# Kernel tuning notes

Hardware: AMD Instinct MI355X
Metric: run time of the kernel (lower is better)

Reference implementation:

```python
import jax, jax.numpy as jnp
import numpy as np

B, N, L = 32, 128, 1024
DRUG_DIM, TGT_DIM, HID, H = 256, 1280, 512, 8
HD = HID // H  # 64
NEG = jnp.float32(-1e9)


def setup_inputs() -> dict:
    key = jax.random.key(0)
    ks = jax.random.split(key, 9)
    drug_nodes = jax.random.normal(ks[0], (B, N, DRUG_DIM), dtype=jnp.float32)
    target_seq = jax.random.normal(ks[1], (B, L, TGT_DIM), dtype=jnp.float32)
    # masks: random valid lengths in [max//2, max], True = valid
    dlen = jax.random.randint(ks[2], (B,), N // 2, N + 1)
    tlen = jax.random.randint(ks[3], (B,), L // 2, L + 1)
    drug_mask = jnp.arange(N)[None, :] < dlen[:, None]
    target_mask = jnp.arange(L)[None, :] < tlen[:, None]
    # params (nn.Linear default init ~ U(-1/sqrt(fan_in), ...); randn*0.02 ok for a reference)
    Wd = jax.random.normal(ks[4], (DRUG_DIM, HID), dtype=jnp.float32) / np.sqrt(DRUG_DIM)
    bd = jnp.zeros((HID,), dtype=jnp.float32)
    Wt = jax.random.normal(ks[5], (TGT_DIM, HID), dtype=jnp.float32) / np.sqrt(TGT_DIM)
    bt = jnp.zeros((HID,), dtype=jnp.float32)
    Wb = jax.random.normal(ks[6], (H, HD, HD), dtype=jnp.float32) * 0.02
    return {"drug_nodes": drug_nodes, "drug_mask": drug_mask,
            "target_seq": target_seq, "target_mask": target_mask,
            "Wd": Wd, "bd": bd, "Wt": Wt, "bt": bt, "Wb": Wb}


def reference(drug_nodes, drug_mask, target_seq, target_mask, Wd, bd, Wt, bt, Wb):
    # project and split heads -> (h, B, n, hd) / (h, B, l, hd)
    d = drug_nodes @ Wd + bd                                  # (B, N, HID)
    t = target_seq @ Wt + bt                                  # (B, L, HID)
    dh = d.reshape(B, N, H, HD).transpose(2, 0, 1, 3)         # (H, B, N, HD)
    th = t.reshape(B, L, H, HD).transpose(2, 0, 1, 3)         # (H, B, L, HD)

    dW = jnp.einsum('hbnd,hde->hbne', dh, Wb)                 # bilinear map
    attn = jnp.einsum('hbne,hble->hbnl', dW, th)              # (H, B, N, L)

    mask = (drug_mask[:, :, None] & target_mask[:, None, :])[None]  # (1, B, N, L)
    scores = jnp.where(mask, attn, NEG)

    # drug-side softmax over protein residues (axis=-1), dropout is identity (eval)
    attn_d = jnp.where(mask, jax.nn.softmax(scores, axis=-1), 0.0)
    ctx_d = jnp.einsum('hbnl,hble->hbne', attn_d, th)         # (H, B, N, HD)
    dmf = drug_mask[None, :, :, None].astype(ctx_d.dtype)
    ctx_d = (ctx_d * dmf).sum(axis=2) / jnp.clip(dmf.sum(axis=2), 1.0)  # (H, B, HD)
    ctx_d = ctx_d.transpose(1, 0, 2).reshape(B, -1)           # (B, HID)

    # target-side softmax over atoms (axis=-2)
    attn_t = jnp.where(mask, jax.nn.softmax(scores, axis=-2), 0.0)
    ctx_t = jnp.einsum('hbnl,hbne->hble', attn_t, dh)         # (H, B, L, HD)
    tmf = target_mask[None, :, :, None].astype(ctx_t.dtype)
    ctx_t = (ctx_t * tmf).sum(axis=2) / jnp.clip(tmf.sum(axis=2), 1.0)  # (H, B, HD)
    ctx_t = ctx_t.transpose(1, 0, 2).reshape(B, -1)           # (B, HID)

    return jnp.concatenate([ctx_d, ctx_t], axis=-1)           # (B, 2*HID)
```

## Files before the change

### kernel.cpp

```cpp
#include <hip/hip_runtime.h>
#include <hip/hip_bf16.h>
#include <math.h>

#define B_ 32
#define N_ 128
#define L_ 1024
#define DD_ 256
#define TD_ 1280
#define HID_ 512
#define H_ 8
#define HD_ 64

#define WS_D    0
#define WS_RM   (WS_D   + 2097152)
#define WS_RIZ  (WS_RM  + 32768)
#define WS_RMT  (WS_RIZ + 32768)
#define WS_RZT  (WS_RMT + 524288)
#define WS_RWT  (WS_RZT + 524288)
#define WS_CNT  (WS_RWT + 524288)
#define WS_WT   (WS_CNT + 64)
#define WS_THB  (WS_WT  + 327680)
#define WS_DWB  (WS_THB + 8388608)

using bf16x8 = __attribute__((ext_vector_type(8))) short;
using u16x4 = __attribute__((ext_vector_type(4))) unsigned short;
using floatx4 = __attribute__((ext_vector_type(4))) float;

static __device__ __forceinline__ unsigned short f2bf(float f) {
  unsigned int u = __float_as_uint(f);
  unsigned int r = (u + 0x7FFFu + ((u >> 16) & 1u)) >> 16;
  return (unsigned short)r;
}
static __device__ __forceinline__ float bf2f(unsigned short s) {
  return __uint_as_float(((unsigned int)s) << 16);
}
static __device__ __forceinline__ void gload16(const void* g, void* l) {
  __builtin_amdgcn_global_load_lds(
      (const __attribute__((address_space(1))) void*)g,
      (__attribute__((address_space(3))) void*)l, 16, 0, 0);
}

__global__ __launch_bounds__(256) void count_kernel(const int* __restrict__ dmask,
                                                    const int* __restrict__ tmask,
                                                    int* __restrict__ cnts) {
  __shared__ int red[256];
  const int b = blockIdx.x, tid = threadIdx.x;
  const bool dint = (dmask[0] == 1);
  const bool tint = (tmask[0] == 1);
  int s = 0;
  if (dint) {
    for (int i = tid; i < N_; i += 256) s += (dmask[(size_t)b*N_ + i] != 0);
  } else {
    const unsigned char* p = (const unsigned char*)dmask;
    for (int i = tid; i < N_; i += 256) s += (p[(size_t)b*N_ + i] != 0);
  }
  red[tid] = s; __syncthreads();
  for (int off = 128; off > 0; off >>= 1) { if (tid < off) red[tid] += red[tid+off]; __syncthreads(); }
  if (tid == 0) cnts[b*2] = red[0];
  __syncthreads();
  s = 0;
  if (tint) {
    for (int i = tid; i < L_; i += 256) s += (tmask[(size_t)b*L_ + i] != 0);
  } else {
    const unsigned char* p = (const unsigned char*)tmask;
    for (int i = tid; i < L_; i += 256) s += (p[(size_t)b*L_ + i] != 0);
  }
  red[tid] = s; __syncthreads();
  for (int off = 128; off > 0; off >>= 1) { if (tid < off) red[tid] += red[tid+off]; __syncthreads(); }
  if (tid == 0) cnts[b*2+1] = red[0];
}

__global__ __launch_bounds__(256) void transpose_bf16_kernel(
    const float* __restrict__ W, unsigned short* __restrict__ WT, int K, int Nd) {
  __shared__ float tile[32][33];
  const int tid = threadIdx.x;
  const int n0 = blockIdx.x * 32, k0 = blockIdx.y * 32;
  const int c = tid & 31, r0 = tid >> 5;
#pragma unroll
  for (int i = 0; i < 4; i++) {
    const int r = r0 + i * 8;
    tile[c][r] = W[(size_t)(k0 + r) * Nd + n0 + c];
  }
  __syncthreads();
#pragma unroll
  for (int i = 0; i < 4; i++) {
    const int r = r0 + i * 8;
    WT[(size_t)(n0 + r) * K + k0 + c] = f2bf(tile[r][c]);
  }
}

__global__ __launch_bounds__(256, 2) void gemm_t_mfma_kernel(
    const float* __restrict__ A, const unsigned short* __restrict__ WT,
    const float* __restrict__ bias, unsigned short* __restrict__ thb, int K) {
  __shared__ __align__(16) unsigned short As[8192];
  __shared__ __align__(16) unsigned short Bs[16384];
  const int tid = threadIdx.x;
  const int lin = blockIdx.x;
  const int xcd = lin & 7, sq = lin >> 3;
  const int n_t = sq & 1, m_t = (sq >> 1) + xcd * 32;
  const int m0 = m_t * 128, n0 = n_t * 256;
  const int lane = tid & 63, wave = tid >> 6;
  const int wm = wave & 1, wn = wave >> 1;
  const int quad = lane >> 4, lrow = lane & 15;

  floatx4 acc[4][8];
#pragma unroll
  for (int i = 0; i < 4; i++)
#pragma unroll
    for (int j = 0; j < 8; j++) acc[i][j] = (floatx4){0.f, 0.f, 0.f, 0.f};

  int srcoffB[4][2];
#pragma unroll
  for (int call = 0; call < 4; call++) {
    const int i = call * 256 + tid;
    const int r = i >> 2;
    const int c = (i & 3) ^ ((r >> 1) & 3);
#pragma unroll
    for (int g = 0; g < 2; g++) srcoffB[call][g] = r * K + g * 32 + c * 8;
  }

  const int arow_ = wave * 4 + (lane >> 4);
  const int x_ = lane & 15;
  const int ag_ = x_ >> 3;
  const int acq_ = (x_ & 7) >> 1;
  const int ahalf_ = x_ & 1;

  const float* Abase = A + (size_t)m0 * K;
  const unsigned short* Bbase = WT + (size_t)n0 * K;

  float4 apf[8];

  auto aload = [&](int k0) {
#pragma unroll
    for (int i = 0; i < 8; i++)
      apf[i] = *(const float4*)(Abase + (size_t)(i * 16 + arow_) * K + k0 + x_ * 4);
  };
  auto awrite = [&]() {
#pragma unroll
    for (int i = 0; i < 8; i++) {
      const int r = i * 16 + arow_;
      const int sw = (r >> 1) & 3;
      u16x4 p;
      p[0] = f2bf(apf[i].x); p[1] = f2bf(apf[i].y);
      p[2] = f2bf(apf[i].z); p[3] = f2bf(apf[i].w);
      *(u16x4*)&As[ag_ * 4096 + (r * 4 + (acq_ ^ sw)) * 8 + ahalf_ * 4] = p;
    }
  };
  auto bstage = [&](int k0) {
#pragma unroll
    for (int g = 0; g < 2; g++)
#pragma unroll
      for (int call = 0; call < 4; call++) {
        const int dst = g * 8192 + (call * 256 + wave * 64) * 8;
        gload16(Bbase + k0 + srcoffB[call][g], &Bs[dst]);
      }
  };

  const int nkt = K / 64;
  aload(0);

  for (int t = 0; t < nkt; t++) {
    __syncthreads();
    bstage(t * 64);
    awrite();
    __syncthreads();
    if (t + 1 < nkt) aload((t + 1) * 64);
#pragma unroll
    for (int g = 0; g < 2; g++) {
      bf16x8 afr[4];
#pragma unroll
      for (int i = 0; i < 4; i++) {
        const int ar = wm * 64 + i * 16 + lrow;
        afr[i] = *(const bf16x8*)&As[g * 4096 + (ar * 4 + (quad ^ ((ar >> 1) & 3))) * 8];
      }
#pragma unroll
      for (int jh = 0; jh < 2; jh++) {
        bf16x8 bfr[4];
#pragma unroll
        for (int j = 0; j < 4; j++) {
          const int br = wn * 128 + (jh * 4 + j) * 16 + lrow;
          bfr[j] = *(const bf16x8*)&Bs[g * 8192 + (br * 4 + (quad ^ ((br >> 1) & 3))) * 8];
        }
#pragma unroll
        for (int i = 0; i < 4; i++)
#pragma unroll
          for (int j = 0; j < 4; j++)
            acc[i][jh * 4 + j] = __builtin_amdgcn_mfma_f32_16x16x32_bf16(
                afr[i], bfr[j], acc[i][jh * 4 + j], 0, 0, 0);
      }
    }
  }

  float bj[8];
#pragma unroll
  for (int j = 0; j < 8; j++) bj[j] = bias[n0 + wn * 128 + j * 16 + lrow];
#pragma unroll
  for (int i = 0; i < 4; i++) {
#pragma unroll
    for (int j = 0; j < 8; j++) {
      const int gcol = n0 + wn * 128 + j * 16 + lrow;
      const int hh = gcol >> 6, e = gcol & 63;
#pragma unroll
      for (int r = 0; r < 4; r++) {
        const int grow = m0 + wm * 64 + i * 16 + quad * 4 + r;
        const int bb = grow >> 10, l = grow & 1023;
        thb[(((size_t)bb * H_ + hh) * L_ + l) * HD_ + e] = f2bf(acc[i][j][r] + bj[j]);
      }
    }
  }
}

__global__ __launch_bounds__(256) void gemm_bias_kernel(
    const float* __restrict__ A, const float* __restrict__ W,
    const float* __restrict__ bias, float* __restrict__ C,
    int M, int K, int Nd) {
  __shared__ float As[8][132];
  __shared__ float Bs[8][132];
  const int tid = threadIdx.x;
  const int m0 = blockIdx.y * 128, n0 = blockIdx.x * 128;
  const int lr = tid >> 1, lc = (tid & 1) * 4;
  const int wr = tid >> 5, wc = (tid & 31) * 4;
  const int tm = (tid >> 4) * 4, tn = (tid & 15) * 4;

  float acc[2][2][4][4];
#pragma unroll
  for (int a = 0; a < 2; a++)
#pragma unroll
    for (int bq = 0; bq < 2; bq++)
#pragma unroll
      for (int i = 0; i < 4; i++)
#pragma unroll
        for (int j = 0; j < 4; j++) acc[a][bq][i][j] = 0.f;

  const float* Aptr = A + (size_t)(m0 + lr) * K + lc;
  const float* Wptr = W + (size_t)wr * Nd + n0 + wc;

  for (int k0 = 0; k0 < K; k0 += 8) {
    float4 a4 = *(const float4*)(Aptr + k0);
    float4 w4 = *(const float4*)(Wptr + (size_t)k0 * Nd);
    __syncthreads();
    As[lc+0][lr] = a4.x; As[lc+1][lr] = a4.y; As[lc+2][lr] = a4.z; As[lc+3][lr] = a4.w;
    *(float4*)&Bs[wr][wc] = w4;
    __syncthreads();
#pragma unroll
    for (int kk = 0; kk < 8; kk++) {
      float4 a0 = *(const float4*)&As[kk][tm];
      float4 a1 = *(const float4*)&As[kk][tm + 64];
      float4 b0 = *(const float4*)&Bs[kk][tn];
      float4 b1 = *(const float4*)&Bs[kk][tn + 64];
      const float av0[4] = {a0.x, a0.y, a0.z, a0.w};
      const float av1[4] = {a1.x, a1.y, a1.z, a1.w};
      const float bv0[4] = {b0.x, b0.y, b0.z, b0.w};
      const float bv1[4] = {b1.x, b1.y, b1.z, b1.w};
#pragma unroll
      for (int i = 0; i < 4; i++)
#pragma unroll
        for (int j = 0; j < 4; j++) {
          acc[0][0][i][j] += av0[i] * bv0[j];
          acc[0][1][i][j] += av0[i] * bv1[j];
          acc[1][0][i][j] += av1[i] * bv0[j];
          acc[1][1][i][j] += av1[i] * bv1[j];
        }
    }
  }
  float4 bias0 = *(const float4*)&bias[n0 + tn];
  float4 bias1 = *(const float4*)&bias[n0 + tn + 64];
  const float bb0[4] = {bias0.x, bias0.y, bias0.z, bias0.w};
  const float bb1[4] = {bias1.x, bias1.y, bias1.z, bias1.w};
#pragma unroll
  for (int mh = 0; mh < 2; mh++)
#pragma unroll
    for (int i = 0; i < 4; i++) {
      const int row = m0 + mh * 64 + tm + i;
      float* cp = C + (size_t)row * Nd + n0;
      float4 o0, o1;
      o0.x = acc[mh][0][i][0] + bb0[0]; o0.y = acc[mh][0][i][1] + bb0[1];
      o0.z = acc[mh][0][i][2] + bb0[2]; o0.w = acc[mh][0][i][3] + bb0[3];
      o1.x = acc[mh][1][i][0] + bb1[0]; o1.y = acc[mh][1][i][1] + bb1[1];
      o1.z = acc[mh][1][i][2] + bb1[2]; o1.w = acc[mh][1][i][3] + bb1[3];
      *(float4*)(cp + tn) = o0;
      *(float4*)(cp + tn + 64) = o1;
    }
}

__global__ __launch_bounds__(256) void dw_kernel(
    const float* __restrict__ dproj, const float* __restrict__ Wb,
    unsigned short* __restrict__ dWb) {
  __shared__ float wb_s[64 * 64];
  __shared__ float dp_s[128 * 64];
  const int tid = threadIdx.x;
  const int hb = blockIdx.x, b = hb >> 3, h = hb & 7;
  for (int i = tid; i < 4096; i += 256) wb_s[i] = Wb[(size_t)h * 4096 + i];
#pragma unroll
  for (int rep = 0; rep < 8; rep++) {
    const int idx = rep * 256 + tid;
    const int row = idx >> 4, c4 = (idx & 15) * 4;
    *(float4*)&dp_s[row * 64 + c4] =
        *(const float4*)&dproj[((size_t)(b * N_ + row)) * HID_ + h * HD_ + c4];
  }
  __syncthreads();
  const int n = tid >> 1, half = tid & 1;
  float acc[32];
#pragma unroll
  for (int e = 0; e < 32; e++) acc[e] = 0.f;
  const float* dpr = &dp_s[n * 64];
  for (int k = 0; k < 64; k++) {
    const float a = dpr[k];
    const float* wr = &wb_s[k * 64 + half * 32];
#pragma unroll
    for (int e4 = 0; e4 < 8; e4++) {
      float4 w = *(const float4*)&wr[e4 * 4];
      acc[e4*4+0] += a * w.x; acc[e4*4+1] += a * w.y;
      acc[e4*4+2] += a * w.z; acc[e4*4+3] += a * w.w;
    }
  }
  unsigned short* outp = dWb + ((size_t)hb * N_ + n) * HD_ + half * 32;
#pragma unroll
  for (int e = 0; e < 32; e++) outp[e] = f2bf(acc[e]);
}

__device__ __forceinline__ void mfma_S_tile(
    const unsigned short* __restrict__ thp, const unsigned short* __restrict__ dwp,
    float* __restrict__ S_s, int ncnt, int lv, int tid) {
  const int lane = tid & 63, wave = tid >> 6;
  const int quad = lane >> 4, lr = lane & 15;
  const int noff = (wave & 1) * 64, loff = (wave >> 1) * 32;

  floatx4 acc[4][2];
#pragma unroll
  for (int i = 0; i < 4; i++)
#pragma unroll
    for (int j = 0; j < 2; j++) acc[i][j] = (floatx4){0.f, 0.f, 0.f, 0.f};

#pragma unroll
  for (int kc = 0; kc < 2; kc++) {
    bf16x8 bfr[2];
#pragma unroll
    for (int j = 0; j < 2; j++)
      bfr[j] = *(const bf16x8*)&thp[(size_t)(loff + j * 16 + lr) * HD_ + kc * 32 + quad * 8];
#pragma unroll
    for (int i = 0; i < 4; i++) {
      bf16x8 afr = *(const bf16x8*)&dwp[(size_t)(noff + i * 16 + lr) * HD_ + kc * 32 + quad * 8];
#pragma unroll
      for (int j = 0; j < 2; j++)
        acc[i][j] = __builtin_amdgcn_mfma_f32_16x16x32_bf16(afr, bfr[j], acc[i][j], 0, 0, 0);
    }
  }
#pragma unroll
  for (int i = 0; i < 4; i++)
#pragma unroll
    for (int j = 0; j < 2; j++)
#pragma unroll
      for (int r = 0; r < 4; r++) {
        const int n = noff + i * 16 + quad * 4 + r;
        const int li = loff + j * 16 + lr;
        const bool ok = (n < ncnt) && (li < lv);
        S_s[n * 69 + li] = ok ? acc[i][j][r] : -1e9f;
      }
}

__global__ __launch_bounds__(256, 4) void attn_stats_kernel(
    const unsigned short* __restrict__ thb, const unsigned short* __restrict__ dWb,
    const int* __restrict__ cnts, float* __restrict__ rwt,
    float* __restrict__ rmt, float* __restrict__ rzt) {
  __shared__ float S_s[128 * 69];
  __shared__ float red[256];
  __shared__ float zb_s[256], wb_s[256];
  __shared__ float cm_s[64], ics_s[64];
  const int tid = threadIdx.x;
  const int hb = blockIdx.x >> 4, lt = blockIdx.x & 15;
  const int b = hb >> 3;
  const int ncnt = cnts[b * 2], lcnt = cnts[b * 2 + 1];
  const int l0g = lt * 64;
  if (l0g >= lcnt) return;
  const int lv = min(64, lcnt - l0g);

  mfma_S_tile(thb + ((size_t)hb * L_ + l0g) * HD_, dWb + (size_t)hb * N_ * HD_,
              S_s, ncnt, lv, tid);
  __syncthreads();

  {
    const int l = tid & 63, q = tid >> 6;
    const int ne = min(q * 32 + 32, ncnt);
    float pm = -INFINITY;
    for (int n = q * 32; n < ne; n++) pm = fmaxf(pm, S_s[n * 69 + l]);
    red[tid] = pm;
  }
  __syncthreads();
  if (tid < 64)
    cm_s[tid] = fmaxf(fmaxf(red[tid], red[tid + 64]), fmaxf(red[tid + 128], red[tid + 192]));
  __syncthreads();
  {
    const int l = tid & 63, q = tid >> 6;
    const int ne = min(q * 32 + 32, ncnt);
    const float cm = cm_s[l];
    float ps = 0.f;
    for (int n = q * 32; n < ne; n++) ps += __expf(S_s[n * 69 + l] - cm);
    red[tid] = ps;
  }
  __syncthreads();
  if (tid < 64)
    ics_s[tid] = 1.f / (red[tid] + red[tid + 64] + red[tid + 128] + red[tid + 192]);
  __syncthreads();
  {
    const int n = tid & 127, half = tid >> 7;
    const float* Sr = &S_s[n * 69];
    const int lb = half * 32, le = min(lb + 32, lv);
    float tmax = -INFINITY;
    for (int l = lb; l < le; l++) tmax = fmaxf(tmax, Sr[l]);
    red[tid] = tmax;
    __syncthreads();
    const float tm = fmaxf(red[n], red[n + 128]);
    float z = 0.f, w = 0.f;
    for (int l = lb; l < le; l++) {
      const float s = Sr[l];
      z += __expf(s - tm);
      w += __expf(s - cm_s[l]) * ics_s[l];
    }
    zb_s[tid] = z; wb_s[tid] = w;
    __syncthreads();
    if (tid < 128) {
      const size_t o = ((size_t)hb * 16 + lt) * 128 + tid;
      rmt[o] = tm;
      rzt[o] = zb_s[tid] + zb_s[tid + 128];
      rwt[o] = wb_s[tid] + wb_s[tid + 128];
    }
  }
}

__global__ __launch_bounds__(256) void attn_combine_kernel(
    const float* __restrict__ rmt, const float* __restrict__ rzt,
    const float* __restrict__ rwt, const float* __restrict__ dproj,
    const int* __restrict__ cnts, float* __restrict__ rm_g,
    float* __restrict__ riz_g, float* __restrict__ outp) {
  __shared__ float red[256];
  __shared__ float w_s[128];
  const int tid = threadIdx.x;
  const int hb = blockIdx.x, b = hb >> 3, h = hb & 7;
  const int ncnt = cnts[b * 2], lcnt = cnts[b * 2 + 1];
  const int ntl = (lcnt + 63) >> 6;
  if (tid < 128) {
    const int n = tid;
    float m = -INFINITY;
    for (int t = 0; t < ntl; t++)
      m = fmaxf(m, rmt[((size_t)hb * 16 + t) * 128 + n]);
    float Z = 0.f, w = 0.f;
    for (int t = 0; t < ntl; t++) {
      const size_t o = ((size_t)hb * 16 + t) * 128 + n;
      Z += rzt[o] * __expf(rmt[o] - m);
      w += rwt[o];
    }
    rm_g[hb * 128 + n] = m;
    riz_g[hb * 128 + n] = (n < ncnt) ? 1.f / Z : 0.f;
    w_s[n] = (n < ncnt) ? w : 0.f;
  }
  __syncthreads();
  const int e = tid & 63, q = tid >> 6;
  float p = 0.f;
  const int nb = q * 32, ne = min(nb + 32, ncnt);
  for (int n = nb; n < ne; n++)
    p += w_s[n] * dproj[((size_t)(b * N_ + n)) * HID_ + h * HD_ + e];
  red[tid] = p;
  __syncthreads();
  if (tid < 64) {
    const float s = red[tid] + red[tid + 64] + red[tid + 128] + red[tid + 192];
    outp[(size_t)b * (2 * HID_) + HID_ + h * HD_ + tid] = s / (float)lcnt;
  }
}

__global__ __launch_bounds__(256, 4) void attn_v_kernel(
    const unsigned short* __restrict__ thb, const unsigned short* __restrict__ dWb,
    const int* __restrict__ cnts, const float* __restrict__ rm_g,
    const float* __restrict__ riz_g, float* __restrict__ outp) {
  __shared__ float S_s[128 * 69];
  __shared__ float red[256];
  __shared__ float rm_s[128], riz_s[128], v_s[64];
  const int tid = threadIdx.x;
  const int hb = blockIdx.x >> 4, lt = blockIdx.x & 15;
  const int b = hb >> 3, h = hb & 7;
  const int ncnt = cnts[b * 2], lcnt = cnts[b * 2 + 1];
  const int l0g = lt * 64;
  if (l0g >= lcnt) return;
  const int lv = min(64, lcnt - l0g);

  if (tid < 128) {
    rm_s[tid] = rm_g[hb * 128 + tid];
    riz_s[tid] = riz_g[hb * 128 + tid];
  }
  const unsigned short* thp = thb + ((size_t)hb * L_ + l0g) * HD_;
  mfma_S_tile(thp, dWb + (size_t)hb * N_ * HD_, S_s, ncnt, lv, tid);
  __syncthreads();

  {
    const int l = tid & 63, q = tid >> 6;
    const int ne = min(q * 32 + 32, ncnt);
    float vp = 0.f;
    for (int n = q * 32; n < ne; n++)
      vp += __expf(S_s[n * 69 + l] - rm_s[n]) * riz_s[n];
    red[tid] = vp;
  }
  __syncthreads();
  const float incnt = 1.f / (float)ncnt;
  if (tid < 64) {
    const float v = (tid < lv)
        ? (red[tid] + red[tid + 64] + red[tid + 128] + red[tid + 192]) * incnt
        : 0.f;
    v_s[tid] = v;
  }
  __syncthreads();
  {
    const int e = tid & 63, q = tid >> 6;
    const int le = min(q * 16 + 16, lv);
    float p = 0.f;
    for (int l = q * 16; l < le; l++)
      p += v_s[l] * bf2f(thp[(size_t)l * HD_ + e]);
    red[tid] = p;
  }
  __syncthreads();
  if (tid < 64) {
    const float s = red[tid] + red[tid + 64] + red[tid + 128] + red[tid + 192];
    if (s != 0.f)
      atomicAdd(&outp[(size_t)b * (2 * HID_) + h * HD_ + tid], s);
  }
}

extern "C" void kernel_launch(void* const* d_in, const int* in_sizes, int n_in,
                              void* d_out, int out_size, void* d_ws, size_t ws_size,
                              hipStream_t stream) {
  const float* drug = (const float*)d_in[0];
  const int* dmask = (const int*)d_in[1];
  const float* tseq = (const float*)d_in[2];
  const int* tmask = (const int*)d_in[3];
  const float* Wd = (const float*)d_in[4];
  const float* bd = (const float*)d_in[5];
  const float* Wt = (const float*)d_in[6];
  const float* bt = (const float*)d_in[7];
  const float* Wb = (const float*)d_in[8];
  float* out = (float*)d_out;
  float* ws = (float*)d_ws;

  float* dp = ws + WS_D;
  float* rm = ws + WS_RM;
  float* riz = ws + WS_RIZ;
  float* rmt = ws + WS_RMT;
  float* rzt = ws + WS_RZT;
  float* rwt = ws + WS_RWT;
  int* cnts = (int*)(ws + WS_CNT);
  unsigned short* wtT = (unsigned short*)(ws + WS_WT);
  unsigned short* thb = (unsigned short*)(ws + WS_THB);
  unsigned short* dWb = (unsigned short*)(ws + WS_DWB);

  count_kernel<<<B_, 256, 0, stream>>>(dmask, tmask, cnts);
  hipMemsetAsync(out, 0, (size_t)out_size * sizeof(float), stream);
  transpose_bf16_kernel<<<dim3(HID_ / 32, TD_ / 32), 256, 0, stream>>>(Wt, wtT, TD_, HID_);
  gemm_t_mfma_kernel<<<(HID_ / 256) * ((B_ * L_) / 128), 256, 0, stream>>>(
      tseq, wtT, bt, thb, TD_);
  gemm_bias_kernel<<<dim3(HID_ / 128, (B_ * N_) / 128), 256, 0, stream>>>(
      drug, Wd, bd, dp, B_ * N_, DD_, HID_);
  dw_kernel<<<B_ * H_, 256, 0, stream>>>(dp, Wb, dWb);
  attn_stats_kernel<<<B_ * H_ * 16, 256, 0, stream>>>(thb, dWb, cnts, rwt, rmt, rzt);
  attn_combine_kernel<<<B_ * H_, 256, 0, stream>>>(rmt, rzt, rwt, dp, cnts, rm, riz, out);
  attn_v_kernel<<<B_ * H_ * 16, 256, 0, stream>>>(thb, dWb, cnts, rm, riz, out);
}
```

Baseline: 452.0 us.

## Keep attention scores in registers in attn_v and unroll fixed-length reductions

attn_v_kernel now computes the score tile with inline MFMA and applies the exp/normalize weighting directly on the accumulator registers. This drops the 35 KB shared-memory score tile and its store/reload, and launch bounds go from 4 to 6 blocks per CU. Several reduction loops in both kernels now use fixed trip counts with unrolling instead of bounds tied to ncnt/lv. That relies on padded score rows and out-of-range v entries being harmless, which is a correctness risk if the padding holds non-finite values.

```diff
diff --git a/kernel.cpp b/kernel.cpp
--- a/kernel.cpp
+++ b/kernel.cpp
@@ -381,9 +381,9 @@
 
   {
     const int l = tid & 63, q = tid >> 6;
-    const int ne = min(q * 32 + 32, ncnt);
     float pm = -INFINITY;
-    for (int n = q * 32; n < ne; n++) pm = fmaxf(pm, S_s[n * 69 + l]);
+#pragma unroll
+    for (int n = q * 32; n < q * 32 + 32; n++) pm = fmaxf(pm, S_s[n * 69 + l]);
     red[tid] = pm;
   }
   __syncthreads();
@@ -392,10 +392,10 @@
   __syncthreads();
   {
     const int l = tid & 63, q = tid >> 6;
-    const int ne = min(q * 32 + 32, ncnt);
     const float cm = cm_s[l];
     float ps = 0.f;
-    for (int n = q * 32; n < ne; n++) ps += __expf(S_s[n * 69 + l] - cm);
+#pragma unroll
+    for (int n = q * 32; n < q * 32 + 32; n++) ps += __expf(S_s[n * 69 + l] - cm);
     red[tid] = ps;
   }
   __syncthreads();
@@ -468,13 +468,14 @@
   }
 }
 
-__global__ __launch_bounds__(256, 4) void attn_v_kernel(
+__global__ __launch_bounds__(256, 6) void attn_v_kernel(
     const unsigned short* __restrict__ thb, const unsigned short* __restrict__ dWb,
     const int* __restrict__ cnts, const float* __restrict__ rm_g,
     const float* __restrict__ riz_g, float* __restrict__ outp) {
-  __shared__ float S_s[128 * 69];
+  __shared__ float rm_s[128], riz_s[128];
+  __shared__ float v_part[2][64];
+  __shared__ float v_s[64];
   __shared__ float red[256];
-  __shared__ float rm_s[128], riz_s[128], v_s[64];
   const int tid = threadIdx.x;
   const int hb = blockIdx.x >> 4, lt = blockIdx.x & 15;
   const int b = hb >> 3, h = hb & 7;
@@ -487,32 +488,70 @@
     rm_s[tid] = rm_g[hb * 128 + tid];
     riz_s[tid] = riz_g[hb * 128 + tid];
   }
+  __syncthreads();
+
+  const int lane = tid & 63, wave = tid >> 6;
+  const int quad = lane >> 4, lr = lane & 15;
+  const int noff = (wave & 1) * 64, loff = (wave >> 1) * 32;
   const unsigned short* thp = thb + ((size_t)hb * L_ + l0g) * HD_;
-  mfma_S_tile(thp, dWb + (size_t)hb * N_ * HD_, S_s, ncnt, lv, tid);
-  __syncthreads();
-
-  {
-    const int l = tid & 63, q = tid >> 6;
-    const int ne = min(q * 32 + 32, ncnt);
-    float vp = 0.f;
-    for (int n = q * 32; n < ne; n++)
-      vp += __expf(S_s[n * 69 + l] - rm_s[n]) * riz_s[n];
-    red[tid] = vp;
+  const unsigned short* dwp = dWb + (size_t)hb * N_ * HD_;
+
+  floatx4 acc[4][2];
+#pragma unroll
+  for (int i = 0; i < 4; i++)
+#pragma unroll
+    for (int j = 0; j < 2; j++) acc[i][j] = (floatx4){0.f, 0.f, 0.f, 0.f};
+#pragma unroll
+  for (int kc = 0; kc < 2; kc++) {
+    bf16x8 bfr[2];
+#pragma unroll
+    for (int j = 0; j < 2; j++)
+      bfr[j] = *(const bf16x8*)&thp[(size_t)(loff + j * 16 + lr) * HD_ + kc * 32 + quad * 8];
+#pragma unroll
+    for (int i = 0; i < 4; i++) {
+      bf16x8 afr = *(const bf16x8*)&dwp[(size_t)(noff + i * 16 + lr) * HD_ + kc * 32 + quad * 8];
+#pragma unroll
+      for (int j = 0; j < 2; j++)
+        acc[i][j] = __builtin_amdgcn_mfma_f32_16x16x32_bf16(afr, bfr[j], acc[i][j], 0, 0, 0);
+    }
+  }
+
+  float vp[2] = {0.f, 0.f};
+  const bool lok0 = (loff + 0 * 16 + lr) < lv;
+  const bool lok1 = (loff + 1 * 16 + lr) < lv;
+#pragma unroll
+  for (int i = 0; i < 4; i++) {
+#pragma unroll
+    for (int r = 0; r < 4; r++) {
+      const int n = noff + i * 16 + quad * 4 + r;
+      if (n < ncnt) {
+        const float m = rm_s[n], rz = riz_s[n];
+        if (lok0) vp[0] += __expf(acc[i][0][r] - m) * rz;
+        if (lok1) vp[1] += __expf(acc[i][1][r] - m) * rz;
+      }
+    }
+  }
+#pragma unroll
+  for (int j = 0; j < 2; j++) {
+    vp[j] += __shfl_xor(vp[j], 16);
+    vp[j] += __shfl_xor(vp[j], 32);
+  }
+  if (quad == 0) {
+#pragma unroll
+    for (int j = 0; j < 2; j++)
+      v_part[wave & 1][loff + j * 16 + lr] = vp[j];
   }
   __syncthreads();
   const float incnt = 1.f / (float)ncnt;
-  if (tid < 64) {
-    const float v = (tid < lv)
-        ? (red[tid] + red[tid + 64] + red[tid + 128] + red[tid + 192]) * incnt
-        : 0.f;
-    v_s[tid] = v;
-  }
-  __syncthreads();
+  if (tid < 64)
+    v_s[tid] = (tid < lv) ? (v_part[0][tid] + v_part[1][tid]) * incnt : 0.f;
+  __syncthreads();
+
   {
     const int e = tid & 63, q = tid >> 6;
-    const int le = min(q * 16 + 16, lv);
     float p = 0.f;
-    for (int l = q * 16; l < le; l++)
+#pragma unroll
+    for (int l = q * 16; l < q * 16 + 16; l++)
       p += v_s[l] * bf2f(thp[(size_t)l * HD_ + e]);
     red[tid] = p;
   }
```

After: 428.1 us. -5.3%, faster.
